# Performance work log

Hardware: AMD Instinct MI355X
Metric: run time of the kernel (lower is better)

The kernel has to match this reference:

```python
import jax, jax.numpy as jnp
import numpy as np

NUM_FEATURES = 16
EMBED_DIM = 8
D = NUM_FEATURES * EMBED_DIM  # 128
BATCH = 524288


def setup_inputs() -> dict:
    key = jax.random.key(0)
    ks = jax.random.split(key, 7)
    s = 1.0 / np.sqrt(D)
    return {
        "x": jax.random.normal(ks[0], (BATCH, D), dtype=jnp.float32),
        "Wk": jax.random.normal(ks[1], (D, D), dtype=jnp.float32) * s,
        "bk": jnp.zeros((D,), dtype=jnp.float32),
        "Wq": jax.random.normal(ks[2], (D, D), dtype=jnp.float32) * s,
        "bq": jnp.zeros((D,), dtype=jnp.float32),
        "Wv": jax.random.normal(ks[3], (D, D), dtype=jnp.float32) * s,
        "bv": jnp.zeros((D,), dtype=jnp.float32),
    }


def reference(x, Wk, bk, Wq, bq, Wv, bv):
    # Dense + exact gelu projections (keras 'gelu' activation is exact erf-gelu)
    gelu = lambda t: jax.nn.gelu(t, approximate=False)
    k = gelu(x @ Wk + bk)  # [B, D]
    q = gelu(x @ Wq + bq)
    v = gelu(x @ Wv + bv)
    B = x.shape[0]
    k = k.reshape(B, NUM_FEATURES, EMBED_DIM)
    q = q.reshape(B, NUM_FEATURES, EMBED_DIM)
    v = v.reshape(B, NUM_FEATURES, EMBED_DIM)
    # y = K^T Q : [B, E, E]; res = V y : [B, F, E]
    y = jnp.einsum('bfe,bfg->beg', k, q)
    res = jnp.einsum('bfe,beg->bfg', v, y)
    return res.reshape(B, D) + x
```

## Files before the change

kernel.cpp:

```cpp
#include <hip/hip_runtime.h>

typedef __bf16 bf16x8 __attribute__((ext_vector_type(8)));
typedef float f32x4 __attribute__((ext_vector_type(4)));
typedef float f32x2 __attribute__((ext_vector_type(2)));
typedef __fp16 fp16x2 __attribute__((ext_vector_type(2)));
typedef unsigned short ushort8 __attribute__((ext_vector_type(8)));
typedef unsigned int uint4v __attribute__((ext_vector_type(4)));
typedef unsigned int uint2v __attribute__((ext_vector_type(2)));

__device__ __forceinline__ unsigned short f2bf(float f){
    unsigned u = __float_as_uint(f);
    u += 0x7fffu + ((u >> 16) & 1u);
    return (unsigned short)(u >> 16);
}
__device__ __forceinline__ unsigned cvt_pk_bf16(float lo, float hi){
    unsigned r;
    asm("v_cvt_pk_bf16_f32 %0, %1, %2" : "=v"(r) : "v"(lo), "v"(hi));
    return r;
}
__device__ __forceinline__ unsigned cvt_pk_f16(float lo, float hi){
    return __builtin_bit_cast(unsigned, __builtin_amdgcn_cvt_pkrtz(lo, hi));
}
__device__ __forceinline__ float fdot2(unsigned a, unsigned b, float c){
#if __has_builtin(__builtin_amdgcn_fdot2)
    return __builtin_amdgcn_fdot2(__builtin_bit_cast(fp16x2, a),
                                  __builtin_bit_cast(fp16x2, b), c, false);
#else
    float d;
    asm("v_dot2_f32_f16 %0, %1, %2, %3" : "=v"(d) : "v"(a), "v"(b), "v"(c));
    return d;
#endif
}
__device__ __forceinline__ float bflo(unsigned w){ return __uint_as_float(w << 16); }
__device__ __forceinline__ float bfhi(unsigned w){ return __uint_as_float(w & 0xffff0000u); }

__device__ __forceinline__ float gelu_poly(float x){
    float t = x * x;
    float h = fmaf(fmaf(fmaf(fmaf(2.66044e-5f, t, -7.46798e-4f), t,
                             9.014181e-3f), t, -6.5889388e-2f), t, 0.39894228f);
    float p = fmaf(x, h, 0.5f);
    p = fminf(fmaxf(p, 0.0f), 1.0f);
    return x * p;
}

#define TM 64
#define LST 136

__global__ void pack_w_kernel(const float* __restrict__ Wk, const float* __restrict__ Wq,
                              const float* __restrict__ Wv, unsigned short* __restrict__ wp){
    int b = blockIdx.x;
    int lane = threadIdx.x;
    int p  = b >> 5;
    int ks = (b >> 3) & 3;
    int nf = b & 7;
    const float* W = (p == 0) ? Wk : ((p == 1) ? Wq : Wv);
    int k0  = ks * 32 + (lane >> 4) * 8;
    int col = nf * 16 + (lane & 15);
    unsigned short* dst = wp + ((size_t)b * 64 + lane) * 8;
    #pragma unroll
    for (int j = 0; j < 8; ++j) dst[j] = f2bf(W[(size_t)(k0 + j) * 128 + col]);
}

__global__ __launch_bounds__(256, 3) void fused_tcross(
        const float* __restrict__ x, const unsigned short* __restrict__ wp,
        const float* __restrict__ bk, const float* __restrict__ bq,
        const float* __restrict__ bv, float* __restrict__ out){
    __shared__ __align__(16) unsigned short smem[3 * TM * LST];

    const int tid  = threadIdx.x;
    const int lane = tid & 63;
    const int wave = tid >> 6;
    const int c16  = lane & 15;
    const int kg   = lane >> 4;
    const long long row0 = (long long)blockIdx.x * TM;

    float bpre0[2], bpre1[2], bpre2[2];
    #pragma unroll
    for (int j = 0; j < 2; ++j){
        int col = (wave * 2 + j) * 16 + c16;
        bpre0[j] = bv[col];
        bpre1[j] = bq[col];
        bpre2[j] = bk[col];
    }

    const float* xblk = x + row0 * 128;
    f32x4 resid[8];
    #pragma unroll
    for (int it = 0; it < 8; ++it){
        int e = wave * 2048 + it * 256 + lane * 4;
        f32x4 v = *(const f32x4*)(xblk + e);
        resid[it] = v;
        uint2v w;
        w[0] = cvt_pk_bf16(v[0], v[1]);
        w[1] = cvt_pk_bf16(v[2], v[3]);
        *(uint2v*)&smem[(e >> 7) * LST + (e & 127)] = w;
    }
    __syncthreads();

    bf16x8 af[4][4];
    #pragma unroll
    for (int m = 0; m < 4; ++m)
        #pragma unroll
        for (int ks = 0; ks < 4; ++ks)
            af[m][ks] = __builtin_bit_cast(bf16x8,
                *(const ushort8*)&smem[(m * 16 + c16) * LST + ks * 32 + kg * 8]);

    const int pack_p[3] = {2, 1, 0};
    #pragma unroll 1
    for (int pi = 0; pi < 3; ++pi){
        f32x4 acc[4][2];
        const f32x4 zero = {0.f, 0.f, 0.f, 0.f};
        #pragma unroll
        for (int m = 0; m < 4; ++m){ acc[m][0] = zero; acc[m][1] = zero; }
        #pragma unroll
        for (int ks = 0; ks < 4; ++ks){
            #pragma unroll
            for (int j = 0; j < 2; ++j){
                const int nf = wave * 2 + j;
                const size_t fidx = ((size_t)((pack_p[pi] * 4 + ks) * 8 + nf) * 64 + lane) * 8;
                bf16x8 wfrag = __builtin_bit_cast(bf16x8, *(const ushort8*)(wp + fidx));
                #pragma unroll
                for (int m = 0; m < 4; ++m)
                    acc[m][j] = __builtin_amdgcn_mfma_f32_16x16x32_bf16(
                        af[m][ks], wfrag, acc[m][j], 0, 0, 0);
            }
        }
        if (pi == 2) __syncthreads();
        unsigned short* sp = smem + (2 - pi) * TM * LST;
        const float bb0 = (pi == 0) ? bpre0[0] : ((pi == 1) ? bpre1[0] : bpre2[0]);
        const float bb1 = (pi == 0) ? bpre0[1] : ((pi == 1) ? bpre1[1] : bpre2[1]);
        #pragma unroll
        for (int j = 0; j < 2; ++j){
            const int col = (wave * 2 + j) * 16 + c16;
            const float bb = j ? bb1 : bb0;
            #pragma unroll
            for (int m = 0; m < 4; ++m){
                float g0 = gelu_poly(acc[m][j][0] + bb);
                float g1 = gelu_poly(acc[m][j][1] + bb);
                float g2 = gelu_poly(acc[m][j][2] + bb);
                float g3 = gelu_poly(acc[m][j][3] + bb);
                unsigned u01 = (pi == 0) ? cvt_pk_f16(g0, g1) : cvt_pk_bf16(g0, g1);
                unsigned u23 = (pi == 0) ? cvt_pk_f16(g2, g3) : cvt_pk_bf16(g2, g3);
                const int r = m * 16 + kg * 4;
                sp[(r + 0) * LST + col] = (unsigned short)u01;
                sp[(r + 1) * LST + col] = (unsigned short)(u01 >> 16);
                sp[(r + 2) * LST + col] = (unsigned short)u23;
                sp[(r + 3) * LST + col] = (unsigned short)(u23 >> 16);
            }
        }
    }
    __syncthreads();

    const int row = tid >> 2;
    const int sub = tid & 3;
    const unsigned short* krow = smem + 0 * TM * LST + row * LST;
    const unsigned short* qrow = smem + 1 * TM * LST + row * LST;
    const unsigned short* vrow = smem + 2 * TM * LST + row * LST;

    f32x2 y2[8];
    #pragma unroll
    for (int e = 0; e < 8; ++e) y2[e] = (f32x2){0.f, 0.f};
    #pragma unroll
    for (int f = 0; f < 16; ++f){
        uint4v ku = *(const uint4v*)(krow + f * 8);
        unsigned qw = *(const unsigned*)(qrow + f * 8 + sub * 2);
        f32x2 qq = {bflo(qw), bfhi(qw)};
        float kf[8] = {bflo(ku[0]), bfhi(ku[0]), bflo(ku[1]), bfhi(ku[1]),
                       bflo(ku[2]), bfhi(ku[2]), bflo(ku[3]), bfhi(ku[3])};
        #pragma unroll
        for (int e = 0; e < 8; ++e){
            f32x2 kk = {kf[e], kf[e]};
            y2[e] += kk * qq;
        }
    }
    unsigned yp0[4], yp1[4];
    #pragma unroll
    for (int i = 0; i < 4; ++i){
        yp0[i] = cvt_pk_f16(y2[2*i][0], y2[2*i+1][0]);
        yp1[i] = cvt_pk_f16(y2[2*i][1], y2[2*i+1][1]);
    }
    f32x2 rr[16];
    #pragma unroll
    for (int f = 0; f < 16; ++f){
        uint4v vv = *(const uint4v*)(vrow + f * 8);
        float a0 = 0.f, a1 = 0.f;
        #pragma unroll
        for (int i = 0; i < 4; ++i){
            a0 = fdot2(vv[i], yp0[i], a0);
            a1 = fdot2(vv[i], yp1[i], a1);
        }
        rr[f] = (f32x2){a0, a1};
    }

    float* s_res = (float*)smem;
    #pragma unroll
    for (int f = 0; f < 16; ++f)
        *(f32x2*)&s_res[row * LST + f * 8 + sub * 2] = rr[f];

    float* outb = out + row0 * 128;
    #pragma unroll
    for (int it = 0; it < 8; ++it){
        int e = wave * 2048 + it * 256 + lane * 4;
        f32x4 rv = *(const f32x4*)&s_res[(e >> 7) * LST + (e & 127)];
        rv += resid[it];
        *(f32x4*)(outb + e) = rv;
    }
}

extern "C" void kernel_launch(void* const* d_in, const int* in_sizes, int n_in,
                              void* d_out, int out_size, void* d_ws, size_t ws_size,
                              hipStream_t stream){
    const float* x  = (const float*)d_in[0];
    const float* Wk = (const float*)d_in[1];
    const float* bk = (const float*)d_in[2];
    const float* Wq = (const float*)d_in[3];
    const float* bq = (const float*)d_in[4];
    const float* Wv = (const float*)d_in[5];
    const float* bv = (const float*)d_in[6];
    float* out = (float*)d_out;
    unsigned short* wp = (unsigned short*)d_ws;

    const int B = in_sizes[0] / 128;

    pack_w_kernel<<<96, 64, 0, stream>>>(Wk, Wq, Wv, wp);
    fused_tcross<<<B / TM, 256, 0, stream>>>(x, wp, bk, bq, bv, out);

    (void)n_in; (void)out_size; (void)ws_size;
}
```

Before: 181.9 us.

## Reuse two LDS planes and defer V projection to raise occupancy

Shrinks shared memory from three planes to two by computing the V projection after K^T Q is reduced, then overwriting the K plane with V. The fp32 residual held in registers is replaced by its bf16 copy, and launch bounds rise from 3 to 4 blocks per CU. The aim is more resident waves to hide global memory latency in this bandwidth-bound kernel. The cost is extra barriers and a bf16-rounded residual add, which lowers output accuracy.

```diff
diff --git a/kernel.cpp b/kernel.cpp
--- a/kernel.cpp
+++ b/kernel.cpp
@@ -45,6 +45,7 @@
 
 #define TM 64
 #define LST 136
+#define PLANE (TM * LST)
 
 __global__ void pack_w_kernel(const float* __restrict__ Wk, const float* __restrict__ Wq,
                               const float* __restrict__ Wv, unsigned short* __restrict__ wp){
@@ -61,11 +62,11 @@
     for (int j = 0; j < 8; ++j) dst[j] = f2bf(W[(size_t)(k0 + j) * 128 + col]);
 }
 
-__global__ __launch_bounds__(256, 3) void fused_tcross(
+__global__ __launch_bounds__(256, 4) void fused_tcross(
         const float* __restrict__ x, const unsigned short* __restrict__ wp,
         const float* __restrict__ bk, const float* __restrict__ bq,
         const float* __restrict__ bv, float* __restrict__ out){
-    __shared__ __align__(16) unsigned short smem[3 * TM * LST];
+    __shared__ __align__(16) unsigned short smem[2 * PLANE];
 
     const int tid  = threadIdx.x;
     const int lane = tid & 63;
@@ -74,25 +75,25 @@
     const int kg   = lane >> 4;
     const long long row0 = (long long)blockIdx.x * TM;
 
-    float bpre0[2], bpre1[2], bpre2[2];
+    float bpk[2], bpq[2], bpv[2];
     #pragma unroll
     for (int j = 0; j < 2; ++j){
         int col = (wave * 2 + j) * 16 + c16;
-        bpre0[j] = bv[col];
-        bpre1[j] = bq[col];
-        bpre2[j] = bk[col];
+        bpk[j] = bk[col];
+        bpq[j] = bq[col];
+        bpv[j] = bv[col];
     }
 
     const float* xblk = x + row0 * 128;
-    f32x4 resid[8];
+    unsigned rbf[16];
     #pragma unroll
     for (int it = 0; it < 8; ++it){
-        int e = wave * 2048 + it * 256 + lane * 4;
+        int e = tid * 4 + it * 1024;
         f32x4 v = *(const f32x4*)(xblk + e);
-        resid[it] = v;
         uint2v w;
         w[0] = cvt_pk_bf16(v[0], v[1]);
         w[1] = cvt_pk_bf16(v[2], v[3]);
+        rbf[2 * it] = w[0]; rbf[2 * it + 1] = w[1];
         *(uint2v*)&smem[(e >> 7) * LST + (e & 127)] = w;
     }
     __syncthreads();
@@ -104,10 +105,10 @@
         for (int ks = 0; ks < 4; ++ks)
             af[m][ks] = __builtin_bit_cast(bf16x8,
                 *(const ushort8*)&smem[(m * 16 + c16) * LST + ks * 32 + kg * 8]);
-
-    const int pack_p[3] = {2, 1, 0};
+    __syncthreads();
+
     #pragma unroll 1
-    for (int pi = 0; pi < 3; ++pi){
+    for (int pi = 0; pi < 2; ++pi){
         f32x4 acc[4][2];
         const f32x4 zero = {0.f, 0.f, 0.f, 0.f};
         #pragma unroll
@@ -117,7 +118,7 @@
             #pragma unroll
             for (int j = 0; j < 2; ++j){
                 const int nf = wave * 2 + j;
-                const size_t fidx = ((size_t)((pack_p[pi] * 4 + ks) * 8 + nf) * 64 + lane) * 8;
+                const size_t fidx = ((size_t)((pi * 4 + ks) * 8 + nf) * 64 + lane) * 8;
                 bf16x8 wfrag = __builtin_bit_cast(bf16x8, *(const ushort8*)(wp + fidx));
                 #pragma unroll
                 for (int m = 0; m < 4; ++m)
@@ -125,22 +126,19 @@
                         af[m][ks], wfrag, acc[m][j], 0, 0, 0);
             }
         }
-        if (pi == 2) __syncthreads();
-        unsigned short* sp = smem + (2 - pi) * TM * LST;
-        const float bb0 = (pi == 0) ? bpre0[0] : ((pi == 1) ? bpre1[0] : bpre2[0]);
-        const float bb1 = (pi == 0) ? bpre0[1] : ((pi == 1) ? bpre1[1] : bpre2[1]);
+        unsigned short* sp = smem + (pi == 0 ? PLANE : 0);
         #pragma unroll
         for (int j = 0; j < 2; ++j){
             const int col = (wave * 2 + j) * 16 + c16;
-            const float bb = j ? bb1 : bb0;
+            const float bb = (pi == 0) ? bpk[j] : bpq[j];
             #pragma unroll
             for (int m = 0; m < 4; ++m){
                 float g0 = gelu_poly(acc[m][j][0] + bb);
                 float g1 = gelu_poly(acc[m][j][1] + bb);
                 float g2 = gelu_poly(acc[m][j][2] + bb);
                 float g3 = gelu_poly(acc[m][j][3] + bb);
-                unsigned u01 = (pi == 0) ? cvt_pk_f16(g0, g1) : cvt_pk_bf16(g0, g1);
-                unsigned u23 = (pi == 0) ? cvt_pk_f16(g2, g3) : cvt_pk_bf16(g2, g3);
+                unsigned u01 = cvt_pk_bf16(g0, g1);
+                unsigned u23 = cvt_pk_bf16(g2, g3);
                 const int r = m * 16 + kg * 4;
                 sp[(r + 0) * LST + col] = (unsigned short)u01;
                 sp[(r + 1) * LST + col] = (unsigned short)(u01 >> 16);
@@ -153,9 +151,8 @@
 
     const int row = tid >> 2;
     const int sub = tid & 3;
-    const unsigned short* krow = smem + 0 * TM * LST + row * LST;
-    const unsigned short* qrow = smem + 1 * TM * LST + row * LST;
-    const unsigned short* vrow = smem + 2 * TM * LST + row * LST;
+    const unsigned short* krow = smem + PLANE + row * LST;
+    const unsigned short* qrow = smem + row * LST;
 
     f32x2 y2[8];
     #pragma unroll
@@ -179,6 +176,53 @@
         yp0[i] = cvt_pk_f16(y2[2*i][0], y2[2*i+1][0]);
         yp1[i] = cvt_pk_f16(y2[2*i][1], y2[2*i+1][1]);
     }
+
+    f32x4 vacc[4][2];
+    {
+        const f32x4 zero = {0.f, 0.f, 0.f, 0.f};
+        #pragma unroll
+        for (int m = 0; m < 4; ++m){ vacc[m][0] = zero; vacc[m][1] = zero; }
+        #pragma unroll
+        for (int ks = 0; ks < 4; ++ks){
+            #pragma unroll
+            for (int j = 0; j < 2; ++j){
+                const int nf = wave * 2 + j;
+                const size_t fidx = ((size_t)((2 * 4 + ks) * 8 + nf) * 64 + lane) * 8;
+                bf16x8 wfrag = __builtin_bit_cast(bf16x8, *(const ushort8*)(wp + fidx));
+                #pragma unroll
+                for (int m = 0; m < 4; ++m)
+                    vacc[m][j] = __builtin_amdgcn_mfma_f32_16x16x32_bf16(
+                        af[m][ks], wfrag, vacc[m][j], 0, 0, 0);
+            }
+        }
+    }
+    __syncthreads();
+
+    {
+        unsigned short* sp = smem + PLANE;
+        #pragma unroll
+        for (int j = 0; j < 2; ++j){
+            const int col = (wave * 2 + j) * 16 + c16;
+            const float bb = bpv[j];
+            #pragma unroll
+            for (int m = 0; m < 4; ++m){
+                float g0 = gelu_poly(vacc[m][j][0] + bb);
+                float g1 = gelu_poly(vacc[m][j][1] + bb);
+                float g2 = gelu_poly(vacc[m][j][2] + bb);
+                float g3 = gelu_poly(vacc[m][j][3] + bb);
+                unsigned u01 = cvt_pk_f16(g0, g1);
+                unsigned u23 = cvt_pk_f16(g2, g3);
+                const int r = m * 16 + kg * 4;
+                sp[(r + 0) * LST + col] = (unsigned short)u01;
+                sp[(r + 1) * LST + col] = (unsigned short)(u01 >> 16);
+                sp[(r + 2) * LST + col] = (unsigned short)u23;
+                sp[(r + 3) * LST + col] = (unsigned short)(u23 >> 16);
+            }
+        }
+    }
+    __syncthreads();
+
+    const unsigned short* vrow = smem + PLANE + row * LST;
     f32x2 rr[16];
     #pragma unroll
     for (int f = 0; f < 16; ++f){
@@ -191,18 +235,21 @@
         }
         rr[f] = (f32x2){a0, a1};
     }
+    __syncthreads();
 
     float* s_res = (float*)smem;
     #pragma unroll
     for (int f = 0; f < 16; ++f)
         *(f32x2*)&s_res[row * LST + f * 8 + sub * 2] = rr[f];
+    __syncthreads();
 
     float* outb = out + row0 * 128;
     #pragma unroll
     for (int it = 0; it < 8; ++it){
-        int e = wave * 2048 + it * 256 + lane * 4;
+        int e = tid * 4 + it * 1024;
         f32x4 rv = *(const f32x4*)&s_res[(e >> 7) * LST + (e & 127)];
-        rv += resid[it];
+        unsigned w0 = rbf[2 * it], w1 = rbf[2 * it + 1];
+        rv += (f32x4){bflo(w0), bfhi(w0), bflo(w1), bfhi(w1)};
         *(f32x4*)(outb + e) = rv;
     }
 }
```

New measurement: 209.6 us. 1.15x slower.
